# Optimization experiments

Hardware: AMD Instinct MI355X
Metric: run time of the kernel (lower is better)

The kernel has to match this reference:

```python
import jax, jax.numpy as jnp
import numpy as np

B, C, H, W = 4, 256, 32, 32
DS, DC, EXP, NSL, NH = 16, 4, 2, 16, 2
DI = EXP * C
DTR = (C + 15) // 16


def layer_norm(x, w, b, eps=1e-5):
    m = x.mean(-1, keepdims=True)
    v = ((x - m) ** 2).mean(-1, keepdims=True)
    return (x - m) / jnp.sqrt(v + eps) * w + b


def conv2d(x, w, b, groups=1, pad=1):
    y = jax.lax.conv_general_dilated(x, w, (1, 1), [(pad, pad), (pad, pad)],
        dimension_numbers=('NCHW', 'OIHW', 'NCHW'), feature_group_count=groups)
    return y + b[None, :, None, None]


def causal_conv1d(x, w, b):
    k = w.shape[-1]
    y = jax.lax.conv_general_dilated(x, w, (1,), [(k - 1, 0)],
        dimension_numbers=('NCH', 'OIH', 'NCH'), feature_group_count=x.shape[1])
    return y + b[None, :, None]


def selective_scan(u, delta, A, Bm, Cm, D, z):
    # u, delta, z: (b,d,l); A: (d,n); Bm, Cm: (b,n,l); D: (d,)
    dA = jnp.exp(jnp.einsum('bdl,dn->lbdn', delta, A))
    dBu = jnp.einsum('bdl,bnl->lbdn', delta * u, Bm)
    Cl = jnp.moveaxis(Cm, -1, 0)  # (l,b,n)
    def step(s, inp):
        dA_t, dBu_t, C_t = inp
        s = dA_t * s + dBu_t
        return s, jnp.einsum('bdn,bn->bd', s, C_t)
    s0 = jnp.zeros(dA.shape[1:], dA.dtype)
    _, ys = jax.lax.scan(step, s0, (dA, dBu, Cl))
    y = jnp.moveaxis(ys, 0, -1) + D[None, :, None] * u
    return y * jax.nn.silu(z)


def mamba_inner(xz, cw, cb, xpw, dtw, dtb, A, D):
    d = xz.shape[1] // 2
    xm, z = xz[:, :d], xz[:, d:]
    xm = jax.nn.silu(causal_conv1d(xm, cw, cb))
    x_dbl = jnp.einsum('bdl,ed->ble', xm, xpw)  # e = dt_rank + 2*d_state
    dt = x_dbl[..., :DTR]
    Bm = x_dbl[..., DTR:DTR + DS]
    Cm = x_dbl[..., DTR + DS:]
    dt = jax.nn.softplus(jnp.einsum('blr,dr->bdl', dt, dtw) + dtb[None, :, None])
    return selective_scan(xm, dt, A, jnp.moveaxis(Bm, -1, 1), jnp.moveaxis(Cm, -1, 1), D, z)


def mamba_v3(hs, in_w, cw, cb, cbw, cbb, csw, csb, xpw, xpbw, xpsw,
             dtw, dtb, dtbw, dtbb, dtsw, dtsb, Alog, Ablog, Aslog, D, Db, Ds, outw):
    b, l, dm = hs.shape
    xz = jnp.einsum('bld,ed->bel', hs, in_w)  # (b, 2*DI, l)
    A, A_b, A_s = -jnp.exp(Alog), -jnp.exp(Ablog), -jnp.exp(Aslog)
    out = mamba_inner(xz, cw, cb, xpw, dtw, dtb, A, D)
    out_b = mamba_inner(xz[:, :, ::-1], cbw, cbb, xpbw, dtbw, dtbb, A_b, Db)
    # slice scan: torch.chunk(nslices,-1) -> stack(-1) -> flatten(-2)
    xz_s = xz.reshape(b, 2 * DI, NSL, l // NSL).transpose(0, 1, 3, 2).reshape(b, 2 * DI, l)
    out_s = mamba_inner(xz_s, csw, csb, xpsw, dtsw, dtsb, A_s, Ds)
    # restore: reshape(b,d,nslices,l//nslices).permute(0,1,3,2).flatten(-2)
    out_s = out_s.reshape(b, DI, NSL, l // NSL).transpose(0, 1, 3, 2).reshape(b, DI, l)
    comb = out + out_b[:, :, ::-1] + out_s
    return jnp.einsum('bdl,od->blo', comb, outw)


def forward(x, proj1_w, proj1_b, proj2_w, proj2_b, norm_w, norm_b,
            q_w, q_b, k_w, k_b, v_w, v_b, o_w, o_b, fc1_w, fc1_b, dw_w, dw_b,
            in_w, cw, cb, cbw, cbb, csw, csb, xpw, xpbw, xpsw,
            dtw, dtb, dtbw, dtbb, dtsw, dtsb, Alog, Ablog, Aslog, D, Db, Ds, outw):
    b, c, h, w = x.shape
    n = h * w
    x_skip = x
    # torch: x.transpose(1,2).reshape(B,C,H,W) -- memory reinterpret, replicated
    x_flat = jnp.transpose(x, (0, 2, 1, 3)).reshape(b, c, h, w)
    xc = conv2d(x_flat, proj1_w, proj1_b)
    xc = jnp.transpose(xc.reshape(b, c, n), (0, 2, 1))
    xc = layer_norm(xc, norm_w, norm_b)
    dh = c // NH
    Q = (xc @ q_w.T + q_b).reshape(b, n, NH, dh).transpose(0, 2, 1, 3)
    K = (xc @ k_w.T + k_b).reshape(b, n, NH, dh).transpose(0, 2, 1, 3)
    V = (xc @ v_w.T + v_b).reshape(b, n, NH, dh).transpose(0, 2, 1, 3)
    scores = jnp.einsum('bhqd,bhkd->bhqk', Q, K) / jnp.sqrt(jnp.float32(dh))
    probs = jax.nn.softmax(scores, axis=-1)
    att = jnp.einsum('bhqk,bhkd->bhqd', probs, V).transpose(0, 2, 1, 3).reshape(b, n, c)
    att = att @ o_w.T + o_b
    # torch: .view(B,C,HW).transpose(1,2) -- memory reinterpret, replicated
    x_att = jnp.transpose(att.reshape(b, c, n), (0, 2, 1))
    xm = mamba_v3(x_att, in_w, cw, cb, cbw, cbb, csw, csb, xpw, xpbw, xpsw,
                  dtw, dtb, dtbw, dtbb, dtsw, dtsb, Alog, Ablog, Aslog, D, Db, Ds, outw)
    xm = jnp.transpose(xm, (0, 2, 1)).reshape(b, c, h, w)
    xm = jax.nn.relu(conv2d(xm, proj1_w, proj1_b))  # proj1 reused (as in source)
    xm = jax.nn.relu(conv2d(xm, proj2_w, proj2_b, pad=0))
    xs = jnp.transpose(xm.reshape(b, c, n), (0, 2, 1))
    xf = xs @ fc1_w.T + fc1_b
    xd = jnp.transpose(xf, (0, 2, 1)).reshape(b, c, h, w)
    xd = conv2d(xd, dw_w, dw_b, groups=c)
    xd = jnp.transpose(xd.reshape(b, c, n), (0, 2, 1))
    out = jnp.transpose(xd.reshape(b, h, w, c), (0, 3, 1, 2)) + x_skip
    return out


def setup_inputs():
    keys = iter(jax.random.split(jax.random.key(0), 64))
    def rn(shape, s=0.02):
        return jax.random.normal(next(keys), shape, jnp.float32) * s
    Alog = jnp.log(jnp.tile(jnp.arange(1, DS + 1, dtype=jnp.float32), (DI, 1)))
    return dict(
        x=jax.random.normal(next(keys), (B, C, H, W), jnp.float32),
        proj1_w=rn((C, C, 3, 3)), proj1_b=jnp.zeros((C,), jnp.float32),
        proj2_w=rn((C, C, 1, 1)), proj2_b=jnp.zeros((C,), jnp.float32),
        norm_w=jnp.ones((C,), jnp.float32), norm_b=jnp.zeros((C,), jnp.float32),
        q_w=rn((C, C)), q_b=jnp.zeros((C,), jnp.float32),
        k_w=rn((C, C)), k_b=jnp.zeros((C,), jnp.float32),
        v_w=rn((C, C)), v_b=jnp.zeros((C,), jnp.float32),
        o_w=rn((C, C)), o_b=jnp.zeros((C,), jnp.float32),
        fc1_w=rn((C, C)), fc1_b=jnp.zeros((C,), jnp.float32),
        dw_w=rn((C, 1, 3, 3)), dw_b=jnp.zeros((C,), jnp.float32),
        in_w=rn((2 * DI, C)),
        cw=rn((DI, 1, DC), 0.1), cb=jnp.zeros((DI,), jnp.float32),
        cbw=rn((DI, 1, DC), 0.1), cbb=jnp.zeros((DI,), jnp.float32),
        csw=rn((DI, 1, DC), 0.1), csb=jnp.zeros((DI,), jnp.float32),
        xpw=rn((DTR + 2 * DS, DI)), xpbw=rn((DTR + 2 * DS, DI)), xpsw=rn((DTR + 2 * DS, DI)),
        dtw=rn((DI, DTR), 0.1), dtb=jnp.full((DI,), -4.6, jnp.float32),
        dtbw=rn((DI, DTR), 0.1), dtbb=jnp.full((DI,), -4.6, jnp.float32),
        dtsw=rn((DI, DTR), 0.1), dtsb=jnp.full((DI,), -4.6, jnp.float32),
        Alog=Alog, Ablog=Alog, Aslog=Alog,
        D=jnp.ones((DI,), jnp.float32), Db=jnp.ones((DI,), jnp.float32), Ds=jnp.ones((DI,), jnp.float32),
        outw=rn((C, DI)),
    )


def reference(x, proj1_w, proj1_b, proj2_w, proj2_b, norm_w, norm_b,
              q_w, q_b, k_w, k_b, v_w, v_b, o_w, o_b, fc1_w, fc1_b, dw_w, dw_b,
              in_w, cw, cb, cbw, cbb, csw, csb, xpw, xpbw, xpsw,
              dtw, dtb, dtbw, dtbb, dtsw, dtsb, Alog, Ablog, Aslog, D, Db, Ds, outw):
    return forward(x, proj1_w, proj1_b, proj2_w, proj2_b, norm_w, norm_b,
                   q_w, q_b, k_w, k_b, v_w, v_b, o_w, o_b, fc1_w, fc1_b, dw_w, dw_b,
                   in_w, cw, cb, cbw, cbb, csw, csb, xpw, xpbw, xpsw,
                   dtw, dtb, dtbw, dtbb, dtsw, dtsb, Alog, Ablog, Aslog, D, Db, Ds, outw)
```

## Files before the change

kernel.cpp:

```cpp
#include <hip/hip_runtime.h>


#define LOG2E 1.4426950408889634f
#define NCH 16
#define LCH 64

typedef unsigned short u16;
typedef unsigned int u32;
typedef __attribute__((ext_vector_type(8))) short bf16x8;
typedef __attribute__((ext_vector_type(4))) float f32x4;

__device__ __forceinline__ u16 f2b(float f) {
  u32 u = __builtin_bit_cast(u32, f);
  u32 r = (u + 0x7fffu + ((u >> 16) & 1u)) >> 16;
  return (u16)r;
}
__device__ __forceinline__ float b2f(u16 h) {
  u32 u = ((u32)h) << 16;
  return __builtin_bit_cast(float, u);
}

#define DPP_ADD(p, ctrl)                                                   \
  (p) += __builtin_bit_cast(float, __builtin_amdgcn_update_dpp(            \
             0, __builtin_bit_cast(int, (p)), ctrl, 0xF, 0xF, true))

static const long BRS = 44544;

struct BrP { const float *cw, *cb, *xpw, *dtw, *dtb, *Al, *Dv; };

__global__ __launch_bounds__(256) void pack_branch_k(float* __restrict__ dst0,
                                                     BrP p0, BrP p1, BrP p2) {
  int z = blockIdx.y;
  BrP p = (z == 0) ? p0 : ((z == 1) ? p1 : p2);
  float* dst = dst0 + (long)z * BRS;
  int t = blockIdx.x * 256 + threadIdx.x;
  if (t < 2048) dst[t] = p.cw[t];
  else if (t < 2560) dst[t] = p.cb[t - 2048];
  else if (t < 27136) dst[t] = p.xpw[t - 2560];
  else if (t < 35328) dst[t] = p.dtw[t - 27136];
  else if (t < 35840) dst[t] = p.dtb[t - 35328];
  else if (t < 44032) dst[t] = -expf(p.Al[t - 35840]) * LOG2E;
  else if (t < 44544) dst[t] = p.Dv[t - 44032];
}

__global__ __launch_bounds__(256) void pack_wb_k(
    const float* __restrict__ qw, const float* __restrict__ kw,
    const float* __restrict__ vw, const float* __restrict__ ow,
    const float* __restrict__ inw, const float* __restrict__ outw,
    const float* __restrict__ p2w, const float* __restrict__ fc1w,
    const float* __restrict__ qb, const float* __restrict__ kb,
    const float* __restrict__ vb, u16* __restrict__ WB,
    float* __restrict__ QBIAS) {
  int t = blockIdx.x * 256 + threadIdx.x;
  if (t < 65536) WB[t] = f2b(qw[t]);
  else if (t < 131072) WB[t] = f2b(kw[t - 65536]);
  else if (t < 196608) WB[t] = f2b(vw[t - 131072]);
  else if (t < 262144) WB[t] = f2b(ow[t - 196608]);
  else if (t < 524288) WB[t] = f2b(inw[t - 262144]);
  else if (t < 655360) WB[t] = f2b(outw[t - 524288]);
  else if (t < 720896) WB[t] = f2b(p2w[t - 655360]);
  else if (t < 786432) WB[t] = f2b(fc1w[t - 720896]);
  else if (t < 787200) {
    int i = t - 786432;
    QBIAS[i] = (i < 256) ? qb[i] : (i < 512 ? kb[i - 256] : vb[i - 512]);
  }
}

__global__ __launch_bounds__(256) void pack_wc_k(const float* __restrict__ w,
                                                 u16* __restrict__ wc) {
  int t = blockIdx.x * 256 + threadIdx.x;
  int ci = t & 255, khw = (t >> 8) % 9, co = t / 2304;
  wc[t] = f2b(w[co * 2304 + ci * 9 + khw]);
}

__global__ __launch_bounds__(256) void xin_k(const float* __restrict__ x,
                                             u16* __restrict__ xin) {
  int t = blockIdx.x * 256 + threadIdx.x;
  int ci = t & 255, w = (t >> 8) & 31, h = (t >> 13) & 31, b = t >> 18;
  int idx = ci * 32 + h;
  xin[t] = f2b(x[((long)b << 18) + ((long)(idx & 255) << 10) +
                 ((idx >> 8) << 5) + w]);
}

__global__ __launch_bounds__(256) void pack_wmb_k(const float* __restrict__ PB,
                                                  u16* __restrict__ WMB,
                                                  float* __restrict__ BIA) {
  int z = blockIdx.y;
  int t = blockIdx.x * 256 + threadIdx.x;
  const float* pb = PB + (long)z * BRS;
  if (t < 16384) {
    int r = t >> 9, k = t & 511;
    WMB[((long)z * 640 + r) * 512 + k] = f2b(pb[2560 + (16 + r) * 512 + k]);
  } else if (t < 65536) {
    int i = t - 16384;
    int r = 544 + (i >> 9), k = i & 511;
    WMB[((long)z * 640 + r) * 512 + k] = 0;
  } else if (t < 66176) {
    int i = t - 65536;
    float v = 0.f;
    if (i >= 32 && i < 544) v = pb[35328 + (i - 32)];
    BIA[(long)z * 640 + i] = v;
  }
}

__global__ __launch_bounds__(256) void pack_wdt_k(const float* __restrict__ PB,
                                                  u16* __restrict__ WMB) {
  int z = blockIdx.y, d = blockIdx.x;
  const float* pb = PB + (long)z * BRS;
  float dtwv[16];
  #pragma unroll
  for (int r = 0; r < 16; ++r) dtwv[r] = pb[27136 + d * 16 + r];
  #pragma unroll
  for (int i = 0; i < 2; ++i) {
    int k = threadIdx.x + i * 256;
    float acc = 0.f;
    #pragma unroll
    for (int r = 0; r < 16; ++r) acc = fmaf(dtwv[r], pb[2560 + r * 512 + k], acc);
    WMB[((long)z * 640 + 32 + d) * 512 + k] = f2b(acc);
  }
}

__global__ __launch_bounds__(256, 2) void conv_mfma_k(
    const u16* __restrict__ in, const u16* __restrict__ wc,
    const float* __restrict__ bias, float* __restrict__ outF,
    u16* __restrict__ outH, int relu) {
  __shared__ u16 ldsA[4][64][8];
  __shared__ u16 ldsB[4][64][8];
  int m0 = blockIdx.x * 64, n0 = blockIdx.y * 64;
  int tid = threadIdx.x;
  int lane = tid & 63, wv = tid >> 6;
  int row = tid & 63, k8 = tid >> 6;
  int l = m0 + row;
  int h = (l >> 5) & 31, w = l & 31;
  int rlo = lane & 15, khl = lane >> 4;
  f32x4 acc[4];
  #pragma unroll
  for (int n = 0; n < 4; ++n) acc[n] = (f32x4){0.f, 0.f, 0.f, 0.f};
  for (int t = 0; t < 72; ++t) {
    int kh = t / 24, r = t % 24, kw = r >> 3, ci0 = (r & 7) << 5;
    __syncthreads();
    bf16x8 av = (bf16x8){0, 0, 0, 0, 0, 0, 0, 0};
    int hh = h + kh - 1, ww = w + kw - 1;
    if ((unsigned)hh < 32u && (unsigned)ww < 32u)
      av = *(const bf16x8*)&in[(long)(l + (kh - 1) * 32 + (kw - 1)) * 256 +
                               ci0 + k8 * 8];
    *(bf16x8*)&ldsA[k8][row][0] = av;
    *(bf16x8*)&ldsB[k8][row][0] =
        *(const bf16x8*)&wc[(long)(n0 + row) * 2304 + t * 32 + k8 * 8];
    __syncthreads();
    bf16x8 af = *(const bf16x8*)&ldsA[khl][wv * 16 + rlo][0];
    #pragma unroll
    for (int n = 0; n < 4; ++n) {
      bf16x8 bf = *(const bf16x8*)&ldsB[khl][n * 16 + rlo][0];
      acc[n] = __builtin_amdgcn_mfma_f32_16x16x32_bf16(af, bf, acc[n], 0, 0, 0);
    }
  }
  int rowb = (lane >> 4) * 4;
  #pragma unroll
  for (int n = 0; n < 4; ++n) {
    int gn = n0 + n * 16 + rlo;
    float bv = bias[gn];
    #pragma unroll
    for (int j = 0; j < 4; ++j) {
      int gm = m0 + wv * 16 + rowb + j;
      float v = acc[n][j] + bv;
      if (relu) v = fmaxf(v, 0.f);
      long oi = (long)gm * 256 + gn;
      if (outH) outH[oi] = f2b(v);
      else outF[oi] = v;
    }
  }
}

__global__ __launch_bounds__(256) void layernorm_k(const float* __restrict__ x,
                                                   const float* __restrict__ w,
                                                   const float* __restrict__ b,
                                                   u16* __restrict__ o) {
  int row = blockIdx.x * 4 + (threadIdx.x >> 6);
  int lane = threadIdx.x & 63;
  float4 v = ((const float4*)(x + (long)row * 256))[lane];
  float s = v.x + v.y + v.z + v.w;
  #pragma unroll
  for (int m = 32; m; m >>= 1) s += __shfl_xor(s, m);
  float mean = s * (1.f / 256.f);
  float4 dv = {v.x - mean, v.y - mean, v.z - mean, v.w - mean};
  float vs = dv.x * dv.x + dv.y * dv.y + dv.z * dv.z + dv.w * dv.w;
  #pragma unroll
  for (int m = 32; m; m >>= 1) vs += __shfl_xor(vs, m);
  float inv = rsqrtf(vs * (1.f / 256.f) + 1e-5f);
  float4 wv = ((const float4*)w)[lane];
  float4 bv = ((const float4*)b)[lane];
  u32 lo = (u32)f2b(dv.x * inv * wv.x + bv.x) |
           ((u32)f2b(dv.y * inv * wv.y + bv.y) << 16);
  u32 hi = (u32)f2b(dv.z * inv * wv.z + bv.z) |
           ((u32)f2b(dv.w * inv * wv.w + bv.w) << 16);
  ((uint2*)(o + (long)row * 256))[lane] = make_uint2(lo, hi);
}

__global__ __launch_bounds__(256) void softmax_k(const float* __restrict__ S,
                                                 u16* __restrict__ P) {
  int row = blockIdx.x * 4 + (threadIdx.x >> 6);
  int lane = threadIdx.x & 63;
  const float4* p = (const float4*)(S + (long)row * 1024);
  float4 v[4];
  float m = -1e30f;
  #pragma unroll
  for (int i = 0; i < 4; ++i) {
    v[i] = p[lane * 4 + i];
    m = fmaxf(m, fmaxf(fmaxf(v[i].x, v[i].y), fmaxf(v[i].z, v[i].w)));
  }
  #pragma unroll
  for (int q = 32; q; q >>= 1) m = fmaxf(m, __shfl_xor(m, q));
  float s = 0.f;
  #pragma unroll
  for (int i = 0; i < 4; ++i) {
    v[i].x = expf(v[i].x - m); v[i].y = expf(v[i].y - m);
    v[i].z = expf(v[i].z - m); v[i].w = expf(v[i].w - m);
    s += v[i].x + v[i].y + v[i].z + v[i].w;
  }
  #pragma unroll
  for (int q = 32; q; q >>= 1) s += __shfl_xor(s, q);
  float inv = 1.f / s;
  uint2* q2 = (uint2*)(P + (long)row * 1024);
  #pragma unroll
  for (int i = 0; i < 4; ++i) {
    u32 lo = (u32)f2b(v[i].x * inv) | ((u32)f2b(v[i].y * inv) << 16);
    u32 hi = (u32)f2b(v[i].z * inv) | ((u32)f2b(v[i].w * inv) << 16);
    q2[lane * 4 + i] = make_uint2(lo, hi);
  }
}

__global__ __launch_bounds__(256, 2) void bgemm_k(
    const u16* __restrict__ A, const u16* __restrict__ B,
    const float* __restrict__ bias, float* __restrict__ OutF,
    u16* __restrict__ OutH, int M, int N, int K,
    int lda, int ldb, int ldo, int zdiv,
    long a_zb, long a_zh, long b_zb, long b_zh, long o_zb, long o_zh,
    float alpha, int act) {
  __shared__ u16 ldsA[4][128][8];
  __shared__ u16 ldsB[4][128][8];
  int z = blockIdx.z, zb = z / zdiv, zh = z - zb * zdiv;
  const u16* Ab = A + zb * a_zb + zh * a_zh;
  const u16* Bb = B + zb * b_zb + zh * b_zh;
  long ob = zb * o_zb + zh * o_zh;
  int m0 = blockIdx.x * 128, n0 = blockIdx.y * 128;
  int tid = threadIdx.x;
  int lane = tid & 63, wv = tid >> 6;
  int wr = wv >> 1, wc = wv & 1;
  int r1 = tid & 127, h1 = tid >> 7;
  int r2 = r1, h2 = h1 + 2;
  const u16* a1 = Ab + (long)(m0 + r1) * lda + h1 * 8;
  const u16* a2 = Ab + (long)(m0 + r2) * lda + h2 * 8;
  const u16* b1 = Bb + (long)(n0 + r1) * ldb + h1 * 8;
  const u16* b2 = Bb + (long)(n0 + r2) * ldb + h2 * 8;

  f32x4 acc[4][4];
  #pragma unroll
  for (int i = 0; i < 4; ++i)
    #pragma unroll
    for (int j = 0; j < 4; ++j) acc[i][j] = (f32x4){0.f, 0.f, 0.f, 0.f};

  bf16x8 ra1 = *(const bf16x8*)a1;
  bf16x8 ra2 = *(const bf16x8*)a2;
  bf16x8 rb1 = *(const bf16x8*)b1;
  bf16x8 rb2 = *(const bf16x8*)b2;

  int nt = K >> 5;
  int kh = lane >> 4, rlo = lane & 15;
  for (int t = 0; t < nt; ++t) {
    __syncthreads();
    *(bf16x8*)&ldsA[h1][r1][0] = ra1;
    *(bf16x8*)&ldsA[h2][r2][0] = ra2;
    *(bf16x8*)&ldsB[h1][r1][0] = rb1;
    *(bf16x8*)&ldsB[h2][r2][0] = rb2;
    if (t + 1 < nt) {
      int ko = (t + 1) << 5;
      ra1 = *(const bf16x8*)(a1 + ko);
      ra2 = *(const bf16x8*)(a2 + ko);
      rb1 = *(const bf16x8*)(b1 + ko);
      rb2 = *(const bf16x8*)(b2 + ko);
    }
    __syncthreads();
    bf16x8 af[4], bfr[4];
    #pragma unroll
    for (int m = 0; m < 4; ++m)
      af[m] = *(const bf16x8*)&ldsA[kh][wr * 64 + m * 16 + rlo][0];
    #pragma unroll
    for (int n = 0; n < 4; ++n)
      bfr[n] = *(const bf16x8*)&ldsB[kh][wc * 64 + n * 16 + rlo][0];
    #pragma unroll
    for (int m = 0; m < 4; ++m)
      #pragma unroll
      for (int n = 0; n < 4; ++n)
        acc[m][n] = __builtin_amdgcn_mfma_f32_16x16x32_bf16(af[m], bfr[n],
                                                            acc[m][n], 0, 0, 0);
  }
  int rowb = (lane >> 4) * 4;
  #pragma unroll
  for (int m = 0; m < 4; ++m) {
    #pragma unroll
    for (int n = 0; n < 4; ++n) {
      int gn = n0 + wc * 64 + n * 16 + rlo;
      float bv = bias ? bias[gn] : 0.f;
      #pragma unroll
      for (int j = 0; j < 4; ++j) {
        int gm = m0 + wr * 64 + m * 16 + rowb + j;
        float v = acc[m][n][j] * alpha + bv;
        if (act == 1) v = fmaxf(v, 0.f);
        long oi = ob + (long)gm * ldo + gn;
        if (OutH) OutH[oi] = f2b(v);
        else OutF[oi] = v;
      }
    }
  }
}

__global__ __launch_bounds__(256, 2) void bgemm64_k(
    const u16* __restrict__ A, const u16* __restrict__ B,
    const float* __restrict__ bias, float* __restrict__ OutF,
    u16* __restrict__ OutH, int M, int N, int K,
    int lda, int ldb, int ldo, int zdiv,
    long a_zb, long a_zh, long b_zb, long b_zh, long o_zb, long o_zh,
    float alpha, int act, int bias_zb, float* __restrict__ Out2,
    const u16* __restrict__ Aux) {
  __shared__ u16 ldsA[4][64][8];
  __shared__ u16 ldsB[4][64][8];
  int z = blockIdx.z, zb = z / zdiv, zh = z - zb * zdiv;
  const u16* Ab = A + zb * a_zb + zh * a_zh;
  const u16* Bb = B + zb * b_zb + zh * b_zh;
  const float* biasb = bias ? bias + (long)zb * bias_zb : nullptr;
  long ob = zb * o_zb + zh * o_zh;
  int m0 = blockIdx.x * 64, n0 = blockIdx.y * 64;
  int tid = threadIdx.x;
  int lane = tid & 63, wv = tid >> 6;
  int row = tid & 63, k8 = tid >> 6;
  int rlo = lane & 15, khl = lane >> 4;
  const u16* pa = Ab + (long)(m0 + row) * lda + k8 * 8;
  const u16* pb = Bb + (long)(n0 + row) * ldb + k8 * 8;
  f32x4 acc[4];
  #pragma unroll
  for (int n = 0; n < 4; ++n) acc[n] = (f32x4){0.f, 0.f, 0.f, 0.f};
  bf16x8 ra = *(const bf16x8*)pa;
  bf16x8 rb = *(const bf16x8*)pb;
  int nt = K >> 5;
  for (int t = 0; t < nt; ++t) {
    __syncthreads();
    *(bf16x8*)&ldsA[k8][row][0] = ra;
    *(bf16x8*)&ldsB[k8][row][0] = rb;
    if (t + 1 < nt) {
      int ko = (t + 1) << 5;
      ra = *(const bf16x8*)(pa + ko);
      rb = *(const bf16x8*)(pb + ko);
    }
    __syncthreads();
    bf16x8 af = *(const bf16x8*)&ldsA[khl][wv * 16 + rlo][0];
    #pragma unroll
    for (int n = 0; n < 4; ++n) {
      bf16x8 bf = *(const bf16x8*)&ldsB[khl][n * 16 + rlo][0];
      acc[n] = __builtin_amdgcn_mfma_f32_16x16x32_bf16(af, bf, acc[n], 0, 0, 0);
    }
  }
  int rowb = (lane >> 4) * 4;
  #pragma unroll
  for (int n = 0; n < 4; ++n) {
    int gn = n0 + n * 16 + rlo;
    float bv = biasb ? biasb[gn] : 0.f;
    #pragma unroll
    for (int j = 0; j < 4; ++j) {
      int gm = m0 + wv * 16 + rowb + j;
      float v = acc[n][j] * alpha + bv;
      if (act == 4) {
        if (gn < 32) {
          Out2[(long)(zb * 4096 + gm) * 32 + gn] = v;
        } else if (gn < 544) {
          float sp = (v > 30.f) ? v : log1pf(expf(v));
          long di = (long)(zb * 4096 + gm) * 512 + (gn - 32);
          ((u32*)OutF)[di] = (u32)f2b(sp) | ((u32)Aux[di] << 16);
        }
      } else {
        if (act == 1) v = fmaxf(v, 0.f);
        long oi = ob + (long)gm * ldo + gn;
        if (OutH) OutH[oi] = f2b(v);
        else OutF[oi] = v;
      }
    }
  }
}

__global__ __launch_bounds__(256) void vt_k(const u16* __restrict__ qkv,
                                            u16* __restrict__ vt) {
  int t = blockIdx.x * 256 + threadIdx.x;
  int j = t & 1023, d = (t >> 10) & 127, bh = t >> 17;
  int b = bh >> 1, h = bh & 1;
  vt[t] = qkv[((long)(b * 1024 + j)) * 768 + 512 + h * 128 + d];
}

__global__ __launch_bounds__(256) void xatt_k(const float* __restrict__ hs,
                                              u16* __restrict__ xa) {
  int t = blockIdx.x * 256 + threadIdx.x;
  int dm = t & 255, l = (t >> 8) & 1023, b = t >> 18;
  xa[t] = f2b(hs[((long)b << 18) + dm * 1024 + l]);
}

__device__ __forceinline__ int brmap(int br, int j) {
  if (br == 0) return j;
  if (br == 1) return 1023 - j;
  return ((j & 15) << 6) | (j >> 4);
}

__global__ __launch_bounds__(256) void cconv_k(const u16* __restrict__ xzb,
                                               const float* __restrict__ pk,
                                               u16* __restrict__ xmcb,
                                               u16* __restrict__ zs) {
  long t = (long)blockIdx.x * 256 + threadIdx.x;
  int d = (int)(t & 511);
  long r = t >> 9;
  int j = (int)(r & 1023);
  int bb = (int)(r >> 10);
  int b = bb & 3, br = bb >> 2;
  const float* pb = pk + (long)br * BRS;
  float acc = pb[2048 + d];
  #pragma unroll
  for (int tap = 0; tap < 4; ++tap) {
    int jj = j - 3 + tap;
    if (jj >= 0) {
      int l = brmap(br, jj);
      acc = fmaf(b2f(xzb[(((long)b << 10) + l) * 1024 + d]), pb[d * 4 + tap],
                 acc);
    }
  }
  float sig = 1.f / (1.f + expf(-acc));
  xmcb[t] = f2b(acc * sig);
  int l = brmap(br, j);
  float zv = b2f(xzb[(((long)b << 10) + l) * 1024 + 512 + d]);
  zs[t] = f2b(zv / (1.f + expf(-zv)));
}

__global__ __launch_bounds__(256) void scanA_k(
    const u32* __restrict__ du, const float* __restrict__ xdbl,
    const float* __restrict__ pk, float* __restrict__ SE,
    float* __restrict__ PC) {
  __shared__ float bs[LCH][16];
  int tid = threadIdx.x;
  int wv = tid >> 6, lane = tid & 63;
  int q = lane & 3, dl = lane >> 2;
  int bb = blockIdx.x >> 3, dch = blockIdx.x & 7;
  int br = bb >> 2, b = bb & 3;
  int d = dch * 64 + wv * 16 + dl;
  int c = blockIdx.y;
  long xdb = (long)br * 131072 + (long)b * 32768 + (long)(c * LCH) * 32;
  {
    int j = tid >> 2, g = tid & 3;
    *(float4*)&bs[j][g * 4] = *(const float4*)&xdbl[xdb + j * 32 + g * 4];
  }
  __syncthreads();
  const float* pb = pk + (long)br * BRS;
  float4 Aln = *(const float4*)&pb[35840 + d * 16 + q * 4];
  long obase = ((long)bb << 19) + (long)(c * LCH) * 512 + d;
  const u32* pdu = du + obase;
  float4 s = {0.f, 0.f, 0.f, 0.f};
  float S = 0.f;
  #pragma unroll 4
  for (int jl = 0; jl < LCH; ++jl) {
    u32 dv = pdu[(long)jl * 512];
    float delta = b2f((u16)dv);
    float uu = b2f((u16)(dv >> 16));
    float w = delta * uu;
    float4 Bv = *(const float4*)&bs[jl][q * 4];
    s.x = fmaf(exp2f(delta * Aln.x), s.x, w * Bv.x);
    s.y = fmaf(exp2f(delta * Aln.y), s.y, w * Bv.y);
    s.z = fmaf(exp2f(delta * Aln.z), s.z, w * Bv.z);
    s.w = fmaf(exp2f(delta * Aln.w), s.w, w * Bv.w);
    S += delta;
  }
  long si = ((((long)bb) * NCH + c) * 512 + d) * 16 + q * 4;
  *(float4*)&SE[si] = s;
  float4 P = {exp2f(Aln.x * S), exp2f(Aln.y * S),
              exp2f(Aln.z * S), exp2f(Aln.w * S)};
  *(float4*)&PC[si] = P;
}

__global__ __launch_bounds__(256) void scanB_k(const float* __restrict__ SE,
                                               const float* __restrict__ PC,
                                               float* __restrict__ SI) {
  long t = (long)blockIdx.x * 256 + threadIdx.x;
  int n = (int)(t & 15);
  int d = (int)((t >> 4) & 511);
  int bb = (int)(t >> 13);
  float run = 0.f;
  for (int c = 0; c < NCH; ++c) {
    long si = (((long)bb * NCH + c) * 512 + d) * 16 + n;
    SI[si] = run;
    run = fmaf(PC[si], run, SE[si]);
  }
}

__global__ __launch_bounds__(256) void scanC_k(
    const u32* __restrict__ du, const float* __restrict__ xdbl,
    const u16* __restrict__ zs, const float* __restrict__ pk,
    const float* __restrict__ SI, u16* __restrict__ y) {
  __shared__ float bcs[LCH][32];
  int tid = threadIdx.x;
  int wv = tid >> 6, lane = tid & 63;
  int q = lane & 3, dl = lane >> 2;
  int bb = blockIdx.x >> 3, dch = blockIdx.x & 7;
  int br = bb >> 2, b = bb & 3;
  int d = dch * 64 + wv * 16 + dl;
  int c = blockIdx.y;
  long xdb = (long)br * 131072 + (long)b * 32768 + (long)(c * LCH) * 32;
  #pragma unroll
  for (int i = 0; i < 2; ++i) {
    int idx = tid + i * 256;
    int j = idx >> 3, g = idx & 7;
    *(float4*)&bcs[j][g * 4] = *(const float4*)&xdbl[xdb + j * 32 + g * 4];
  }
  __syncthreads();
  const float* pb = pk + (long)br * BRS;
  float4 Aln = *(const float4*)&pb[35840 + d * 16 + q * 4];
  float Dv = pb[44032 + d];
  long obase = ((long)bb << 19) + (long)(c * LCH) * 512 + d;
  long si = ((((long)bb) * NCH + c) * 512 + d) * 16 + q * 4;
  float4 s = *(const float4*)&SI[si];
  const u32* pdu = du + obase;
  const u16* pzs = zs + obase;
  u16* py = y + obase;
  #pragma unroll 4
  for (int jl = 0; jl < LCH; ++jl) {
    u32 dv = pdu[(long)jl * 512];
    float delta = b2f((u16)dv);
    float uu = b2f((u16)(dv >> 16));
    float w = delta * uu;
    float4 Bv = *(const float4*)&bcs[jl][q * 4];
    float4 Cv = *(const float4*)&bcs[jl][16 + q * 4];
    s.x = fmaf(exp2f(delta * Aln.x), s.x, w * Bv.x);
    s.y = fmaf(exp2f(delta * Aln.y), s.y, w * Bv.y);
    s.z = fmaf(exp2f(delta * Aln.z), s.z, w * Bv.z);
    s.w = fmaf(exp2f(delta * Aln.w), s.w, w * Bv.w);
    float p = s.x * Cv.x;
    p = fmaf(s.y, Cv.y, p);
    p = fmaf(s.z, Cv.z, p);
    p = fmaf(s.w, Cv.w, p);
    DPP_ADD(p, 0xB1);
    DPP_ADD(p, 0x4E);
    if (q == 0)
      py[(long)jl * 512] = f2b((p + Dv * uu) * b2f(pzs[(long)jl * 512]));
  }
}

__global__ __launch_bounds__(256) void combine_k(const u16* __restrict__ y,
                                                 u16* __restrict__ comb) {
  long t = (long)blockIdx.x * 256 + threadIdx.x;
  int d = (int)(t & 511);
  long r = t >> 9;
  int l = (int)(r & 1023);
  int b = (int)(r >> 10);
  int j2 = ((l & 63) << 4) | (l >> 6);
  float v = b2f(y[(((long)b << 10) + l) * 512 + d])
          + b2f(y[(((long)(4 + b) << 10) + (1023 - l)) * 512 + d])
          + b2f(y[(((long)(8 + b) << 10) + j2) * 512 + d]);
  comb[t] = f2b(v);
}

__global__ __launch_bounds__(256) void dw_k(const u16* __restrict__ xfb,
                                            const float* __restrict__ dww,
                                            const float* __restrict__ dwb,
                                            const float* __restrict__ x,
                                            float* __restrict__ out) {
  __shared__ float plane[1024];
  int bc = blockIdx.x;
  int b = bc >> 8, c = bc & 255;
  int tid = threadIdx.x;
  #pragma unroll
  for (int i = 0; i < 4; ++i) {
    int n = tid + i * 256;
    plane[n] = b2f(xfb[(((long)b << 10) + n) * 256 + c]);
  }
  __syncthreads();
  float wv[9];
  #pragma unroll
  for (int k = 0; k < 9; ++k) wv[k] = dww[c * 9 + k];
  float bb = dwb[c];
  long obase = ((long)(b * 256 + c)) << 10;
  #pragma unroll
  for (int i = 0; i < 4; ++i) {
    int n = tid + i * 256;
    int h = n >> 5, w = n & 31;
    float acc = bb;
    #pragma unroll
    for (int kh = 0; kh < 3; ++kh) {
      int hh = h + kh - 1;
      if ((unsigned)hh >= 32u) continue;
      #pragma unroll
      for (int kw = 0; kw < 3; ++kw) {
        int ww = w + kw - 1;
        if ((unsigned)ww >= 32u) continue;
        acc = fmaf(plane[hh * 32 + ww], wv[kh * 3 + kw], acc);
      }
    }
    out[obase + n] = acc + x[obase + n];
  }
}

extern "C" void kernel_launch(void* const* d_in, const int* in_sizes, int n_in,
                              void* d_out, int out_size, void* d_ws, size_t ws_size,
                              hipStream_t stream) {
  (void)in_sizes; (void)n_in; (void)out_size; (void)ws_size;
  const float* x    = (const float*)d_in[0];
  const float* p1w  = (const float*)d_in[1];
  const float* p1b  = (const float*)d_in[2];
  const float* p2w  = (const float*)d_in[3];
  const float* p2b  = (const float*)d_in[4];
  const float* nw   = (const float*)d_in[5];
  const float* nb   = (const float*)d_in[6];
  const float* qw   = (const float*)d_in[7];
  const float* qb   = (const float*)d_in[8];
  const float* kw   = (const float*)d_in[9];
  const float* kb   = (const float*)d_in[10];
  const float* vw   = (const float*)d_in[11];
  const float* vb   = (const float*)d_in[12];
  const float* ow   = (const float*)d_in[13];
  const float* ob   = (const float*)d_in[14];
  const float* fc1w = (const float*)d_in[15];
  const float* fc1b = (const float*)d_in[16];
  const float* dww  = (const float*)d_in[17];
  const float* dwb  = (const float*)d_in[18];
  const float* inw  = (const float*)d_in[19];
  const float* cw   = (const float*)d_in[20];
  const float* cb   = (const float*)d_in[21];
  const float* cbw  = (const float*)d_in[22];
  const float* cbb  = (const float*)d_in[23];
  const float* csw  = (const float*)d_in[24];
  const float* csb  = (const float*)d_in[25];
  const float* xpw  = (const float*)d_in[26];
  const float* xpbw = (const float*)d_in[27];
  const float* xpsw = (const float*)d_in[28];
  const float* dtw  = (const float*)d_in[29];
  const float* dtb  = (const float*)d_in[30];
  const float* dtbw = (const float*)d_in[31];
  const float* dtbb = (const float*)d_in[32];
  const float* dtsw = (const float*)d_in[33];
  const float* dtsb = (const float*)d_in[34];
  const float* Alog = (const float*)d_in[35];
  const float* Ablog= (const float*)d_in[36];
  const float* Aslog= (const float*)d_in[37];
  const float* Dv   = (const float*)d_in[38];
  const float* Dbv  = (const float*)d_in[39];
  const float* Dsv  = (const float*)d_in[40];
  const float* outw = (const float*)d_in[41];
  float* out = (float*)d_out;

  float* ws    = (float*)d_ws;
  float* PB    = ws;
  u16*   WCONV = (u16*)(ws + 140000);
  u16*   WB    = (u16*)(ws + 440000);
  float* QBIAS = ws + 840000;
  u16*   XINB  = (u16*)(ws + 850000);
  float* R     = ws + 1400000;

  u16*    XZB  = (u16*)R;
  u32*    DUB  = (u32*)R;
  u16*    Y    = (u16*)(R + 6400000);
  u16*    ZS   = (u16*)(R + 12600000);
  float*  SE   = R + 15750000;
  float*  PC   = R + 17350000;
  float*  SI   = R + 19000000;
  u16*    XMCB = (u16*)(R + 22050000);
  u16*   COMBB = (u16*)(R + 23750000);
  float*  XDBL = R + 25200000;
  u16*    WMB  = (u16*)(R + 25600000);
  float*  BIA  = R + 26100000;
  float* XCT   = R + 4300000;
  u16*   XCTB  = (u16*)(R + 5400000);
  u16*   QKVB  = (u16*)(R + 6000000);
  u16*   VT    = (u16*)(R + 7600000);
  float* SC    = R + 8200000;
  u16*   P     = (u16*)(R + 16600000);
  u16*   ATTB  = (u16*)(R + 20900000);
  float* HS    = R + 21500000;
  u16*   XATTB = (u16*)(R + 22600000);
  u16*   XMBB  = (u16*)R;
  u16*   XM2B  = (u16*)(R + 600000);
  u16*   XPB   = (u16*)(R + 1200000);
  u16*   XFB   = (u16*)(R + 1800000);

  u16* WQKVB = WB;
  u16* OWB   = WB + 196608;
  u16* INWB  = WB + 262144;
  u16* OUTWB = WB + 524288;
  u16* P2WB  = WB + 655360;
  u16* FC1WB = WB + 720896;

  auto bgemm = [&](const u16* A, const u16* Bm, const float* bias,
                   float* OutF, u16* OutH, int M, int N, int K,
                   int lda, int ldb, int ldo, int nz, int zdiv,
                   long a_zb, long a_zh, long b_zb, long b_zh,
                   long o_zb, long o_zh, float alpha, int act) {
    dim3 g(M / 128, N / 128, nz);
    bgemm_k<<<g, 256, 0, stream>>>(A, Bm, bias, OutF, OutH, M, N, K,
                                   lda, ldb, ldo, zdiv, a_zb, a_zh,
                                   b_zb, b_zh, o_zb, o_zh, alpha, act);
  };
  auto bgemm64 = [&](const u16* A, const u16* Bm, const float* bias,
                     float* OutF, u16* OutH, int M, int N, int K,
                     int lda, int ldb, int ldo, int nz, int zdiv,
                     long a_zb, long a_zh, long b_zb, long b_zh,
                     long o_zb, long o_zh, float alpha, int act,
                     int bias_zb, float* Out2, const u16* Aux) {
    dim3 g(M / 64, N / 64, nz);
    bgemm64_k<<<g, 256, 0, stream>>>(A, Bm, bias, OutF, OutH, M, N, K,
                                     lda, ldb, ldo, zdiv, a_zb, a_zh,
                                     b_zb, b_zh, o_zb, o_zh, alpha, act,
                                     bias_zb, Out2, Aux);
  };

  BrP b0 = {cw, cb, xpw, dtw, dtb, Alog, Dv};
  BrP b1 = {cbw, cbb, xpbw, dtbw, dtbb, Ablog, Dbv};
  BrP b2 = {csw, csb, xpsw, dtsw, dtsb, Aslog, Dsv};
  pack_branch_k<<<dim3(174, 3), 256, 0, stream>>>(PB, b0, b1, b2);
  pack_wb_k<<<3075, 256, 0, stream>>>(qw, kw, vw, ow, inw, outw, p2w, fc1w,
                                      qb, kb, vb, WB, QBIAS);
  pack_wc_k<<<2304, 256, 0, stream>>>(p1w, WCONV);
  xin_k<<<4096, 256, 0, stream>>>(x, XINB);
  pack_wmb_k<<<dim3(259, 3), 256, 0, stream>>>(PB, WMB, BIA);
  pack_wdt_k<<<dim3(512, 3), 256, 0, stream>>>(PB, WMB);

  conv_mfma_k<<<dim3(64, 4), 256, 0, stream>>>(XINB, WCONV, p1b, XCT, nullptr, 0);
  layernorm_k<<<1024, 256, 0, stream>>>(XCT, nw, nb, XCTB);

  bgemm64(XCTB, WQKVB, QBIAS, nullptr, QKVB, 4096, 768, 256, 256, 256, 768,
          1, 1, 0, 0, 0, 0, 0, 0, 1.f, 0, 0, nullptr, nullptr);
  vt_k<<<4096, 256, 0, stream>>>(QKVB, VT);

  bgemm(QKVB, QKVB + 256, nullptr, SC, nullptr, 1024, 1024, 128, 768, 768, 1024,
        8, 2, 786432, 128, 786432, 128, 2097152, 1048576,
        0.08838834764831845f, 0);
  softmax_k<<<2048, 256, 0, stream>>>(SC, P);

  bgemm64(P, VT, nullptr, nullptr, ATTB, 1024, 128, 1024, 1024, 1024, 256,
          8, 2, 2097152, 1048576, 262144, 131072, 262144, 128, 1.f, 0,
          0, nullptr, nullptr);

  bgemm64(ATTB, OWB, ob, HS, nullptr, 4096, 256, 256, 256, 256, 256,
          1, 1, 0, 0, 0, 0, 0, 0, 1.f, 0, 0, nullptr, nullptr);
  xatt_k<<<4096, 256, 0, stream>>>(HS, XATTB);

  bgemm64(XATTB, INWB, nullptr, nullptr, XZB, 1024, 1024, 256, 256, 256, 1024,
          4, 1, 262144, 0, 0, 0, 1048576, 0, 1.f, 0, 0, nullptr, nullptr);

  cconv_k<<<24576, 256, 0, stream>>>(XZB, PB, XMCB, ZS);

  bgemm64(XMCB, WMB, BIA, (float*)DUB, nullptr, 4096, 576, 512, 512, 512, 0,
          3, 1, 2097152, 0, 327680, 0, 0, 0, 1.f, 4, 640, XDBL, XMCB);

  scanA_k<<<dim3(96, NCH), 256, 0, stream>>>(DUB, XDBL, PB, SE, PC);
  scanB_k<<<384, 256, 0, stream>>>(SE, PC, SI);
  scanC_k<<<dim3(96, NCH), 256, 0, stream>>>(DUB, XDBL, ZS, PB, SI, Y);

  combine_k<<<8192, 256, 0, stream>>>(Y, COMBB);

  bgemm64(COMBB, OUTWB, nullptr, nullptr, XMBB, 4096, 256, 512, 512, 512, 256,
          1, 1, 0, 0, 0, 0, 0, 0, 1.f, 0, 0, nullptr, nullptr);

  conv_mfma_k<<<dim3(64, 4), 256, 0, stream>>>(XMBB, WCONV, p1b, nullptr, XM2B, 1);

  bgemm64(XM2B, P2WB, p2b, nullptr, XPB, 4096, 256, 256, 256, 256, 256,
          1, 1, 0, 0, 0, 0, 0, 0, 1.f, 1, 0, nullptr, nullptr);

  bgemm64(XPB, FC1WB, fc1b, nullptr, XFB, 4096, 256, 256, 256, 256, 256,
          1, 1, 0, 0, 0, 0, 0, 0, 1.f, 0, 0, nullptr, nullptr);

  dw_k<<<1024, 256, 0, stream>>>(XFB, dww, dwb, x, out);
}
```

Measured before the change: 543.3 us.

## Drop scanB and 128-tile GEMM, unpack delta/u streams in scan kernels

Removes the separate inter-chunk prefix kernel (scanB). scanC now rebuilds its starting state by serially combining SE/PC over all earlier chunks. The scores GEMM now uses the 64-tile bgemm kernel instead of the 128-tile one. The x_proj GEMM epilogue writes softplus(dt) as plain bf16 rather than interleaving it with u, so the scans read dt and u from two separate arrays. This saves a launch and the SI buffer, but adds redundant prefix work in later chunks, extra strided loads in the scans, and a lower-reuse tiling for the score GEMM.

New measurement: 552.5 us. Within noise of the previous version (+1.7%).

```diff
diff --git a/kernel.cpp b/kernel.cpp
--- a/kernel.cpp
+++ b/kernel.cpp
@@ -94,7 +94,7 @@
   } else if (t < 65536) {
     int i = t - 16384;
     int r = 544 + (i >> 9), k = i & 511;
-    WMB[((long)z * 640 + r) * 512 + k] = 0;
+    if (r < 640) WMB[((long)z * 640 + r) * 512 + k] = 0;
   } else if (t < 66176) {
     int i = t - 65536;
     float v = 0.f;
@@ -230,99 +230,13 @@
   }
 }
 
-__global__ __launch_bounds__(256, 2) void bgemm_k(
-    const u16* __restrict__ A, const u16* __restrict__ B,
-    const float* __restrict__ bias, float* __restrict__ OutF,
-    u16* __restrict__ OutH, int M, int N, int K,
-    int lda, int ldb, int ldo, int zdiv,
-    long a_zb, long a_zh, long b_zb, long b_zh, long o_zb, long o_zh,
-    float alpha, int act) {
-  __shared__ u16 ldsA[4][128][8];
-  __shared__ u16 ldsB[4][128][8];
-  int z = blockIdx.z, zb = z / zdiv, zh = z - zb * zdiv;
-  const u16* Ab = A + zb * a_zb + zh * a_zh;
-  const u16* Bb = B + zb * b_zb + zh * b_zh;
-  long ob = zb * o_zb + zh * o_zh;
-  int m0 = blockIdx.x * 128, n0 = blockIdx.y * 128;
-  int tid = threadIdx.x;
-  int lane = tid & 63, wv = tid >> 6;
-  int wr = wv >> 1, wc = wv & 1;
-  int r1 = tid & 127, h1 = tid >> 7;
-  int r2 = r1, h2 = h1 + 2;
-  const u16* a1 = Ab + (long)(m0 + r1) * lda + h1 * 8;
-  const u16* a2 = Ab + (long)(m0 + r2) * lda + h2 * 8;
-  const u16* b1 = Bb + (long)(n0 + r1) * ldb + h1 * 8;
-  const u16* b2 = Bb + (long)(n0 + r2) * ldb + h2 * 8;
-
-  f32x4 acc[4][4];
-  #pragma unroll
-  for (int i = 0; i < 4; ++i)
-    #pragma unroll
-    for (int j = 0; j < 4; ++j) acc[i][j] = (f32x4){0.f, 0.f, 0.f, 0.f};
-
-  bf16x8 ra1 = *(const bf16x8*)a1;
-  bf16x8 ra2 = *(const bf16x8*)a2;
-  bf16x8 rb1 = *(const bf16x8*)b1;
-  bf16x8 rb2 = *(const bf16x8*)b2;
-
-  int nt = K >> 5;
-  int kh = lane >> 4, rlo = lane & 15;
-  for (int t = 0; t < nt; ++t) {
-    __syncthreads();
-    *(bf16x8*)&ldsA[h1][r1][0] = ra1;
-    *(bf16x8*)&ldsA[h2][r2][0] = ra2;
-    *(bf16x8*)&ldsB[h1][r1][0] = rb1;
-    *(bf16x8*)&ldsB[h2][r2][0] = rb2;
-    if (t + 1 < nt) {
-      int ko = (t + 1) << 5;
-      ra1 = *(const bf16x8*)(a1 + ko);
-      ra2 = *(const bf16x8*)(a2 + ko);
-      rb1 = *(const bf16x8*)(b1 + ko);
-      rb2 = *(const bf16x8*)(b2 + ko);
-    }
-    __syncthreads();
-    bf16x8 af[4], bfr[4];
-    #pragma unroll
-    for (int m = 0; m < 4; ++m)
-      af[m] = *(const bf16x8*)&ldsA[kh][wr * 64 + m * 16 + rlo][0];
-    #pragma unroll
-    for (int n = 0; n < 4; ++n)
-      bfr[n] = *(const bf16x8*)&ldsB[kh][wc * 64 + n * 16 + rlo][0];
-    #pragma unroll
-    for (int m = 0; m < 4; ++m)
-      #pragma unroll
-      for (int n = 0; n < 4; ++n)
-        acc[m][n] = __builtin_amdgcn_mfma_f32_16x16x32_bf16(af[m], bfr[n],
-                                                            acc[m][n], 0, 0, 0);
-  }
-  int rowb = (lane >> 4) * 4;
-  #pragma unroll
-  for (int m = 0; m < 4; ++m) {
-    #pragma unroll
-    for (int n = 0; n < 4; ++n) {
-      int gn = n0 + wc * 64 + n * 16 + rlo;
-      float bv = bias ? bias[gn] : 0.f;
-      #pragma unroll
-      for (int j = 0; j < 4; ++j) {
-        int gm = m0 + wr * 64 + m * 16 + rowb + j;
-        float v = acc[m][n][j] * alpha + bv;
-        if (act == 1) v = fmaxf(v, 0.f);
-        long oi = ob + (long)gm * ldo + gn;
-        if (OutH) OutH[oi] = f2b(v);
-        else OutF[oi] = v;
-      }
-    }
-  }
-}
-
 __global__ __launch_bounds__(256, 2) void bgemm64_k(
     const u16* __restrict__ A, const u16* __restrict__ B,
     const float* __restrict__ bias, float* __restrict__ OutF,
     u16* __restrict__ OutH, int M, int N, int K,
     int lda, int ldb, int ldo, int zdiv,
     long a_zb, long a_zh, long b_zb, long b_zh, long o_zb, long o_zh,
-    float alpha, int act, int bias_zb, float* __restrict__ Out2,
-    const u16* __restrict__ Aux) {
+    float alpha, int act, int bias_zb, float* __restrict__ Out2) {
   __shared__ u16 ldsA[4][64][8];
   __shared__ u16 ldsB[4][64][8];
   int z = blockIdx.z, zb = z / zdiv, zh = z - zb * zdiv;
@@ -374,8 +288,7 @@
           Out2[(long)(zb * 4096 + gm) * 32 + gn] = v;
         } else if (gn < 544) {
           float sp = (v > 30.f) ? v : log1pf(expf(v));
-          long di = (long)(zb * 4096 + gm) * 512 + (gn - 32);
-          ((u32*)OutF)[di] = (u32)f2b(sp) | ((u32)Aux[di] << 16);
+          OutH[(long)(zb * 4096 + gm) * 512 + (gn - 32)] = f2b(sp);
         }
       } else {
         if (act == 1) v = fmaxf(v, 0.f);
@@ -437,9 +350,9 @@
 }
 
 __global__ __launch_bounds__(256) void scanA_k(
-    const u32* __restrict__ du, const float* __restrict__ xdbl,
-    const float* __restrict__ pk, float* __restrict__ SE,
-    float* __restrict__ PC) {
+    const u16* __restrict__ dt, const u16* __restrict__ um,
+    const float* __restrict__ xdbl, const float* __restrict__ pk,
+    float* __restrict__ SE, float* __restrict__ PC) {
   __shared__ float bs[LCH][16];
   int tid = threadIdx.x;
   int wv = tid >> 6, lane = tid & 63;
@@ -457,14 +370,14 @@
   const float* pb = pk + (long)br * BRS;
   float4 Aln = *(const float4*)&pb[35840 + d * 16 + q * 4];
   long obase = ((long)bb << 19) + (long)(c * LCH) * 512 + d;
-  const u32* pdu = du + obase;
+  const u16* pdt = dt + obase;
+  const u16* pum = um + obase;
   float4 s = {0.f, 0.f, 0.f, 0.f};
   float S = 0.f;
   #pragma unroll 4
   for (int jl = 0; jl < LCH; ++jl) {
-    u32 dv = pdu[(long)jl * 512];
-    float delta = b2f((u16)dv);
-    float uu = b2f((u16)(dv >> 16));
+    float delta = b2f(pdt[(long)jl * 512]);
+    float uu = b2f(pum[(long)jl * 512]);
     float w = delta * uu;
     float4 Bv = *(const float4*)&bs[jl][q * 4];
     s.x = fmaf(exp2f(delta * Aln.x), s.x, w * Bv.x);
@@ -480,25 +393,11 @@
   *(float4*)&PC[si] = P;
 }
 
-__global__ __launch_bounds__(256) void scanB_k(const float* __restrict__ SE,
-                                               const float* __restrict__ PC,
-                                               float* __restrict__ SI) {
-  long t = (long)blockIdx.x * 256 + threadIdx.x;
-  int n = (int)(t & 15);
-  int d = (int)((t >> 4) & 511);
-  int bb = (int)(t >> 13);
-  float run = 0.f;
-  for (int c = 0; c < NCH; ++c) {
-    long si = (((long)bb * NCH + c) * 512 + d) * 16 + n;
-    SI[si] = run;
-    run = fmaf(PC[si], run, SE[si]);
-  }
-}
-
 __global__ __launch_bounds__(256) void scanC_k(
-    const u32* __restrict__ du, const float* __restrict__ xdbl,
-    const u16* __restrict__ zs, const float* __restrict__ pk,
-    const float* __restrict__ SI, u16* __restrict__ y) {
+    const u16* __restrict__ dt, const u16* __restrict__ um,
+    const float* __restrict__ xdbl, const u16* __restrict__ zs,
+    const float* __restrict__ pk, const float* __restrict__ SE,
+    const float* __restrict__ PC, u16* __restrict__ y) {
   __shared__ float bcs[LCH][32];
   int tid = threadIdx.x;
   int wv = tid >> 6, lane = tid & 63;
@@ -519,16 +418,24 @@
   float4 Aln = *(const float4*)&pb[35840 + d * 16 + q * 4];
   float Dv = pb[44032 + d];
   long obase = ((long)bb << 19) + (long)(c * LCH) * 512 + d;
-  long si = ((((long)bb) * NCH + c) * 512 + d) * 16 + q * 4;
-  float4 s = *(const float4*)&SI[si];
-  const u32* pdu = du + obase;
+  float4 s = {0.f, 0.f, 0.f, 0.f};
+  for (int cp = 0; cp < c; ++cp) {
+    long sic = ((((long)bb) * NCH + cp) * 512 + d) * 16 + q * 4;
+    float4 se = *(const float4*)&SE[sic];
+    float4 pc = *(const float4*)&PC[sic];
+    s.x = fmaf(pc.x, s.x, se.x);
+    s.y = fmaf(pc.y, s.y, se.y);
+    s.z = fmaf(pc.z, s.z, se.z);
+    s.w = fmaf(pc.w, s.w, se.w);
+  }
+  const u16* pdt = dt + obase;
+  const u16* pum = um + obase;
   const u16* pzs = zs + obase;
   u16* py = y + obase;
   #pragma unroll 4
   for (int jl = 0; jl < LCH; ++jl) {
-    u32 dv = pdu[(long)jl * 512];
-    float delta = b2f((u16)dv);
-    float uu = b2f((u16)(dv >> 16));
+    float delta = b2f(pdt[(long)jl * 512]);
+    float uu = b2f(pum[(long)jl * 512]);
     float w = delta * uu;
     float4 Bv = *(const float4*)&bcs[jl][q * 4];
     float4 Cv = *(const float4*)&bcs[jl][16 + q * 4];
@@ -658,12 +565,11 @@
   float* R     = ws + 1400000;
 
   u16*    XZB  = (u16*)R;
-  u32*    DUB  = (u32*)R;
+  u16*    DT   = (u16*)R;
   u16*    Y    = (u16*)(R + 6400000);
   u16*    ZS   = (u16*)(R + 12600000);
   float*  SE   = R + 15750000;
   float*  PC   = R + 17350000;
-  float*  SI   = R + 19000000;
   u16*    XMCB = (u16*)(R + 22050000);
   u16*   COMBB = (u16*)(R + 23750000);
   float*  XDBL = R + 25200000;
@@ -690,27 +596,17 @@
   u16* P2WB  = WB + 655360;
   u16* FC1WB = WB + 720896;
 
-  auto bgemm = [&](const u16* A, const u16* Bm, const float* bias,
-                   float* OutF, u16* OutH, int M, int N, int K,
-                   int lda, int ldb, int ldo, int nz, int zdiv,
-                   long a_zb, long a_zh, long b_zb, long b_zh,
-                   long o_zb, long o_zh, float alpha, int act) {
-    dim3 g(M / 128, N / 128, nz);
-    bgemm_k<<<g, 256, 0, stream>>>(A, Bm, bias, OutF, OutH, M, N, K,
-                                   lda, ldb, ldo, zdiv, a_zb, a_zh,
-                                   b_zb, b_zh, o_zb, o_zh, alpha, act);
-  };
   auto bgemm64 = [&](const u16* A, const u16* Bm, const float* bias,
                      float* OutF, u16* OutH, int M, int N, int K,
                      int lda, int ldb, int ldo, int nz, int zdiv,
                      long a_zb, long a_zh, long b_zb, long b_zh,
                      long o_zb, long o_zh, float alpha, int act,
-                     int bias_zb, float* Out2, const u16* Aux) {
+                     int bias_zb, float* Out2) {
     dim3 g(M / 64, N / 64, nz);
     bgemm64_k<<<g, 256, 0, stream>>>(A, Bm, bias, OutF, OutH, M, N, K,
                                      lda, ldb, ldo, zdiv, a_zb, a_zh,
                                      b_zb, b_zh, o_zb, o_zh, alpha, act,
-                                     bias_zb, Out2, Aux);
+                                     bias_zb, Out2);
   };
 
   BrP b0 = {cw, cb, xpw, dtw, dtb, Alog, Dv};
@@ -728,46 +624,45 @@
   layernorm_k<<<1024, 256, 0, stream>>>(XCT, nw, nb, XCTB);
 
   bgemm64(XCTB, WQKVB, QBIAS, nullptr, QKVB, 4096, 768, 256, 256, 256, 768,
-          1, 1, 0, 0, 0, 0, 0, 0, 1.f, 0, 0, nullptr, nullptr);
+          1, 1, 0, 0, 0, 0, 0, 0, 1.f, 0, 0, nullptr);
   vt_k<<<4096, 256, 0, stream>>>(QKVB, VT);
 
-  bgemm(QKVB, QKVB + 256, nullptr, SC, nullptr, 1024, 1024, 128, 768, 768, 1024,
-        8, 2, 786432, 128, 786432, 128, 2097152, 1048576,
-        0.08838834764831845f, 0);
+  bgemm64(QKVB, QKVB + 256, nullptr, SC, nullptr, 1024, 1024, 128, 768, 768,
+          1024, 8, 2, 786432, 128, 786432, 128, 2097152, 1048576,
+          0.08838834764831845f, 0, 0, nullptr);
   softmax_k<<<2048, 256, 0, stream>>>(SC, P);
 
   bgemm64(P, VT, nullptr, nullptr, ATTB, 1024, 128, 1024, 1024, 1024, 256,
           8, 2, 2097152, 1048576, 262144, 131072, 262144, 128, 1.f, 0,
-          0, nullptr, nullptr);
+          0, nullptr);
 
   bgemm64(ATTB, OWB, ob, HS, nullptr, 4096, 256, 256, 256, 256, 256,
-          1, 1, 0, 0, 0, 0, 0, 0, 1.f, 0, 0, nullptr, nullptr);
+          1, 1, 0, 0, 0, 0, 0, 0, 1.f, 0, 0, nullptr);
   xatt_k<<<4096, 256, 0, stream>>>(HS, XATTB);
 
   bgemm64(XATTB, INWB, nullptr, nullptr, XZB, 1024, 1024, 256, 256, 256, 1024,
-          4, 1, 262144, 0, 0, 0, 1048576, 0, 1.f, 0, 0, nullptr, nullptr);
+          4, 1, 262144, 0, 0, 0, 1048576, 0, 1.f, 0, 0, nullptr);
 
   cconv_k<<<24576, 256, 0, stream>>>(XZB, PB, XMCB, ZS);
 
-  bgemm64(XMCB, WMB, BIA, (float*)DUB, nullptr, 4096, 576, 512, 512, 512, 0,
-          3, 1, 2097152, 0, 327680, 0, 0, 0, 1.f, 4, 640, XDBL, XMCB);
-
-  scanA_k<<<dim3(96, NCH), 256, 0, stream>>>(DUB, XDBL, PB, SE, PC);
-  scanB_k<<<384, 256, 0, stream>>>(SE, PC, SI);
-  scanC_k<<<dim3(96, NCH), 256, 0, stream>>>(DUB, XDBL, ZS, PB, SI, Y);
+  bgemm64(XMCB, WMB, BIA, nullptr, DT, 4096, 576, 512, 512, 512, 0,
+          3, 1, 2097152, 0, 327680, 0, 0, 0, 1.f, 4, 640, XDBL);
+
+  scanA_k<<<dim3(96, NCH), 256, 0, stream>>>(DT, XMCB, XDBL, PB, SE, PC);
+  scanC_k<<<dim3(96, NCH), 256, 0, stream>>>(DT, XMCB, XDBL, ZS, PB, SE, PC, Y);
 
   combine_k<<<8192, 256, 0, stream>>>(Y, COMBB);
 
   bgemm64(COMBB, OUTWB, nullptr, nullptr, XMBB, 4096, 256, 512, 512, 512, 256,
-          1, 1, 0, 0, 0, 0, 0, 0, 1.f, 0, 0, nullptr, nullptr);
+          1, 1, 0, 0, 0, 0, 0, 0, 1.f, 0, 0, nullptr);
 
   conv_mfma_k<<<dim3(64, 4), 256, 0, stream>>>(XMBB, WCONV, p1b, nullptr, XM2B, 1);
 
   bgemm64(XM2B, P2WB, p2b, nullptr, XPB, 4096, 256, 256, 256, 256, 256,
-          1, 1, 0, 0, 0, 0, 0, 0, 1.f, 1, 0, nullptr, nullptr);
+          1, 1, 0, 0, 0, 0, 0, 0, 1.f, 1, 0, nullptr);
 
   bgemm64(XPB, FC1WB, fc1b, nullptr, XFB, 4096, 256, 256, 256, 256, 256,
-          1, 1, 0, 0, 0, 0, 0, 0, 1.f, 0, 0, nullptr, nullptr);
+          1, 1, 0, 0, 0, 0, 0, 0, 1.f, 0, 0, nullptr);
 
   dw_k<<<1024, 256, 0, stream>>>(XFB, dww, dwb, x, out);
 }
```
